# Kernel optimization log

Hardware: AMD Instinct MI355X
Metric: run time of the kernel (lower is better)

Reference implementation:

```python
import jax, jax.numpy as jnp
import numpy as np

EMBED_DIM = 512
NUM_HEADS = 8
GLOBAL_MIX = 0.5


def setup_inputs() -> dict:
    key = jax.random.key(0)
    ks = jax.random.split(key, 7)
    B, L, E = 8, 1024, EMBED_DIM
    s = 1.0 / np.sqrt(E)
    x = jax.random.normal(ks[0], (B, L, E), dtype=jnp.float32)
    mask = jax.random.randint(ks[1], (B, L), 0, 2) > 0  # True = valid token
    Wq = jax.random.normal(ks[2], (E, E), dtype=jnp.float32) * s
    Wk = jax.random.normal(ks[3], (E, E), dtype=jnp.float32) * s
    Wv = jax.random.normal(ks[4], (E, E), dtype=jnp.float32) * s
    Wo = jax.random.normal(ks[5], (E, E), dtype=jnp.float32) * s
    G = jax.random.normal(ks[6], (L, L), dtype=jnp.float32)
    return {"x": x, "mask": mask, "Wq": Wq, "Wk": Wk, "Wv": Wv, "Wo": Wo, "G": G}


def _tanh_mha(x, mask, Wq, Wk, Wv, Wo, G):
    B, L, E = x.shape
    H = NUM_HEADS
    D = E // H
    scale = 1.0 / np.sqrt(D)
    dt = x.dtype
    fmax = jnp.finfo(dt).max
    tiny = jnp.finfo(dt).tiny

    def split_heads(t):  # (B,L,E) -> (B,H,L,D)
        return t.reshape(B, L, H, D).transpose(0, 2, 1, 3)

    q = split_heads(x @ Wq.T)
    k = split_heads(x @ Wk.T)
    v = split_heads(x @ Wv.T)

    scores = jnp.tanh(jnp.einsum('bhqd,bhkd->bhqk', q, k) * scale)
    key_valid = mask[:, None, None, :]  # (B,1,1,L)
    scores = jnp.where(key_valid, scores, -jnp.inf)

    finite = jnp.isfinite(scores)
    finite_scores = jnp.where(finite, scores, -fmax)
    m = jnp.max(finite_scores, axis=(1, 2, 3), keepdims=True)  # per-sample amax over heads+q+k
    m = jnp.where(jnp.isfinite(m), m, jnp.zeros_like(m))
    exp_scores = jnp.where(finite, jnp.exp(scores - m), jnp.zeros_like(scores))

    mf = mask.astype(dt)
    exp_scores = exp_scores * mf[:, None, None, :] * mf[:, None, :, None]
    denom = jnp.maximum(exp_scores.sum(axis=(1, 2, 3), keepdims=True), tiny)
    weights = exp_scores / denom
    # dropout p=0 -> identity; renorm pass kept for faithfulness
    renorm = jnp.maximum(weights.sum(axis=(1, 2, 3), keepdims=True), tiny)
    weights = weights / renorm

    # learnable global attention: softmax rows, clamp, mask, normalize over (q,k)
    activated = jnp.maximum(jax.nn.softmax(G, axis=-1), 0.0)  # (L,L)
    gscores = activated[None] * mf[:, None, :] * mf[:, :, None]  # (B,L,L)
    gsums = jnp.maximum(gscores.sum(axis=(1, 2), keepdims=True), tiny)
    gnorm = (gscores / gsums)[:, None]  # (B,1,L,L)
    weights = (1.0 - GLOBAL_MIX) * weights + GLOBAL_MIX * gnorm

    attended = jnp.einsum('bhqk,bhkd->bhqd', weights, v)
    attended = attended * mf[:, None, :, None]
    attended = attended.transpose(0, 2, 1, 3).reshape(B, L, E)
    return attended @ Wo.T


def reference(x, mask, Wq, Wk, Wv, Wo, G):
    return _tanh_mha(x, mask, Wq, Wk, Wv, Wo, G)
```

## Files before the change

### kernel.cpp

```cpp
#include <hip/hip_runtime.h>
#include <math.h>

#define B_ 8
#define L_ 1024
#define E_ 512
#define H_ 8
#define D_ 64
#define QSZ (B_*H_*L_*D_)
#define BLE ((size_t)B_*L_*E_)
#define TINYF 1.175494350822287508e-38f
#define SWK(r) ((((r) ^ ((r) >> 3))) & 7)

typedef unsigned short u16;
typedef __attribute__((ext_vector_type(8))) short bfrag;
typedef __attribute__((ext_vector_type(4))) float ffrag;
typedef __attribute__((ext_vector_type(16))) float ffrag16;
typedef __attribute__((ext_vector_type(4))) short vshort4;

#if __has_builtin(__builtin_amdgcn_exp2f)
#define EXP2F(x) __builtin_amdgcn_exp2f(x)
#else
#define EXP2F(x) __expf((x) * 0.6931471805599453f)
#endif
#if __has_builtin(__builtin_amdgcn_rcpf)
#define RCPF(x) __builtin_amdgcn_rcpf(x)
#else
#define RCPF(x) (1.0f / (x))
#endif

__device__ __forceinline__ u16 f2b(float f) {
  unsigned u = __float_as_uint(f);
  u += 0x7fffu + ((u >> 16) & 1u);
  return (u16)(u >> 16);
}
__device__ __forceinline__ unsigned pk2(float a, float b) {
  unsigned ua = __float_as_uint(a); ua += 0x7fffu + ((ua >> 16) & 1u);
  unsigned ub = __float_as_uint(b); ub += 0x7fffu + ((ub >> 16) & 1u);
  return (ua >> 16) | (ub & 0xffff0000u);
}
__device__ __forceinline__ float blo(unsigned u) { return __uint_as_float(u << 16); }
__device__ __forceinline__ float bhi(unsigned u) { return __uint_as_float(u & 0xffff0000u); }

__device__ __forceinline__ bfrag cvt8v(const float* __restrict__ src) {
  float4 a = *(const float4*)src;
  float4 b = *(const float4*)(src + 4);
  bfrag r;
  r[0]=(short)f2b(a.x); r[1]=(short)f2b(a.y); r[2]=(short)f2b(a.z); r[3]=(short)f2b(a.w);
  r[4]=(short)f2b(b.x); r[5]=(short)f2b(b.y); r[6]=(short)f2b(b.z); r[7]=(short)f2b(b.w);
  return r;
}

__device__ __forceinline__ void gll16(const void* g, void* l) {
  __builtin_amdgcn_global_load_lds(
      (const __attribute__((address_space(1))) void*)g,
      (__attribute__((address_space(3))) void*)l, 16, 0, 0);
}

__global__ __launch_bounds__(256) void prep_softmax_k(
    const float* __restrict__ x, const float* __restrict__ Wq,
    const float* __restrict__ Wk, const float* __restrict__ Wv,
    const float* __restrict__ Wo, const float* __restrict__ G,
    const int* __restrict__ mask,
    u16* __restrict__ xb, u16* __restrict__ Wb, u16* __restrict__ actb,
    float* __restrict__ R, int* __restrict__ posb, int* __restrict__ nvb,
    int* __restrict__ itok) {
  const int bid = blockIdx.x, t = threadIdx.x;
  __shared__ float sred[8];
  __shared__ float rred[4][8];
  __shared__ int sc[256];
  if (bid < 2048) {
    size_t c = (size_t)bid * 256 + t;
    *(bfrag*)&xb[c * 8] = cvt8v(x + c * 8);
    return;
  }
  if (bid < 2560) {
    const int c2 = bid - 2048;
    const float* src = (c2 < 128) ? Wq : (c2 < 256) ? Wk : (c2 < 384) ? Wv : Wo;
    const size_t base = (size_t)(c2 >> 7) * 262144;
    const size_t cc = (size_t)(c2 & 127) * 256 + t;
    *(bfrag*)&Wb[base + cc * 8] = cvt8v(src + cc * 8);
    return;
  }
  if (bid >= 3584) {
    const int bb = bid - 3584;
    int4 mi = *(const int4*)(mask + bb * 1024 + t * 4);
    const int vx = mi.x ? 1 : 0, vy = mi.y ? 1 : 0;
    const int vz = mi.z ? 1 : 0, vw = mi.w ? 1 : 0;
    const int c0 = vx + vy + vz + vw;
    sc[t] = c0;
    __syncthreads();
#pragma unroll
    for (int off = 1; off < 256; off <<= 1) {
      int v = (t >= off) ? sc[t - off] : 0;
      __syncthreads();
      sc[t] += v;
      __syncthreads();
    }
    const int nvtot = sc[255];
    int pv = sc[t] - c0;
    int pi = t * 4 - pv;
    int4 pq;
    pq.x = vx ? pv : nvtot + pi; pv += vx; pi += 1 - vx;
    pq.y = vy ? pv : nvtot + pi; pv += vy; pi += 1 - vy;
    pq.z = vz ? pv : nvtot + pi; pv += vz; pi += 1 - vz;
    pq.w = vw ? pv : nvtot + pi;
    *(int4*)(posb + bb * 1024 + t * 4) = pq;
    itok[bb * 1024 + pq.x] = t * 4;
    itok[bb * 1024 + pq.y] = t * 4 + 1;
    itok[bb * 1024 + pq.z] = t * 4 + 2;
    itok[bb * 1024 + pq.w] = t * 4 + 3;
    if (t == 0) nvb[bb] = nvtot;
    return;
  }
  const int q = bid - 2560;
  const int w = t >> 6, lane = t & 63;
  float4 g4 = ((const float4*)(G + (size_t)q * 1024))[t];
  float m = fmaxf(fmaxf(g4.x, g4.y), fmaxf(g4.z, g4.w));
#pragma unroll
  for (int off = 32; off > 0; off >>= 1) m = fmaxf(m, __shfl_down(m, off));
  if (lane == 0) sred[w] = m;
  __syncthreads();
  m = fmaxf(fmaxf(sred[0], sred[1]), fmaxf(sred[2], sred[3]));
  float e0 = __expf(g4.x - m), e1 = __expf(g4.y - m);
  float e2 = __expf(g4.z - m), e3 = __expf(g4.w - m);
  float s = e0 + e1 + e2 + e3;
#pragma unroll
  for (int off = 32; off > 0; off >>= 1) s += __shfl_down(s, off);
  if (lane == 0) sred[4 + w] = s;
  __syncthreads();
  const float inv = 1.0f / (sred[4] + sred[5] + sred[6] + sred[7]);
  const unsigned p0 = pk2(e0 * inv, e1 * inv);
  const unsigned p1 = pk2(e2 * inv, e3 * inv);
  *(uint2*)&actb[(size_t)q * 1024 + t * 4] = make_uint2(p0, p1);
  const float r0 = blo(p0), r1 = bhi(p0);
  const float r2 = blo(p1), r3 = bhi(p1);
  float rd[8];
#pragma unroll
  for (int b = 0; b < 8; ++b) {
    const int* mkp = mask + b * 1024 + t * 4;
    rd[b] = (mkp[0] ? r0 : 0.f) + (mkp[1] ? r1 : 0.f) +
            (mkp[2] ? r2 : 0.f) + (mkp[3] ? r3 : 0.f);
#pragma unroll
    for (int off = 32; off > 0; off >>= 1) rd[b] += __shfl_down(rd[b], off);
  }
  if (lane == 0)
#pragma unroll
    for (int b = 0; b < 8; ++b) rred[w][b] = rd[b];
  __syncthreads();
  if (t < 8) R[q * 8 + t] = rred[0][t] + rred[1][t] + rred[2][t] + rred[3][t];
}

__global__ __launch_bounds__(256) void proj_k(
    const u16* __restrict__ xb, const u16* __restrict__ Wb,
    const int* __restrict__ mask, const float* __restrict__ R,
    const int* __restrict__ posb,
    float* __restrict__ sums,
    u16* __restrict__ Qb, u16* __restrict__ Kb, u16* __restrict__ Vtb) {
  const int m0 = blockIdx.x * 128;
  const int n0 = blockIdx.y * 128;
  __shared__ __align__(16) u16 As[128 * 64];
  __shared__ __align__(16) u16 Bs[128 * 64];
  __shared__ float rr[4][8];
  const int t = threadIdx.x, w = t >> 6, lane = t & 63;
  const int l15 = lane & 15, quad = lane >> 4;
  const int mq = (w >> 1) * 64, nq = (w & 1) * 64;

  if (blockIdx.x == 0 && blockIdx.y == 0) {
    float a8[8] = {0,0,0,0,0,0,0,0};
    for (int q = t; q < 1024; q += 256)
#pragma unroll
      for (int b = 0; b < 8; ++b)
        if (mask[b * 1024 + q]) a8[b] += R[q * 8 + b];
#pragma unroll
    for (int b = 0; b < 8; ++b) {
#pragma unroll
      for (int off = 32; off > 0; off >>= 1) a8[b] += __shfl_down(a8[b], off);
    }
    if (lane == 0)
#pragma unroll
      for (int b = 0; b < 8; ++b) rr[w][b] = a8[b];
    __syncthreads();
    if (t < 8) {
      sums[t] = 0.0f;
      sums[8 + t] = rr[0][t] + rr[1][t] + rr[2][t] + rr[3][t];
    }
  }

  const ffrag fz = {0.f, 0.f, 0.f, 0.f};
  ffrag acc[4][4];
#pragma unroll
  for (int i = 0; i < 4; ++i)
#pragma unroll
    for (int j = 0; j < 4; ++j) acc[i][j] = fz;

  for (int kk = 0; kk < 512; kk += 64) {
    __syncthreads();
#pragma unroll
    for (int j = 0; j < 4; ++j) {
      const int c = w * 256 + j * 64 + lane;
      const int row = c >> 3, ck = (c & 7) ^ (row & 7);
      gll16(xb + (size_t)(m0 + row) * 512 + kk + ck * 8,
            &As[(size_t)(w * 256 + j * 64) * 8]);
    }
#pragma unroll
    for (int j = 0; j < 4; ++j) {
      const int c = w * 256 + j * 64 + lane;
      const int row = c >> 3, ck = (c & 7) ^ (row & 7);
      gll16(Wb + (size_t)(n0 + row) * 512 + kk + ck * 8,
            &Bs[(size_t)(w * 256 + j * 64) * 8]);
    }
    __syncthreads();
#pragma unroll
    for (int s = 0; s < 2; ++s) {
      bfrag av[4], bv[4];
#pragma unroll
      for (int i = 0; i < 4; ++i) {
        const int ar = mq + i * 16 + l15;
        av[i] = *(const bfrag*)&As[ar * 64 + (((quad + 4 * s) ^ (ar & 7)) << 3)];
        const int br = nq + i * 16 + l15;
        bv[i] = *(const bfrag*)&Bs[br * 64 + (((quad + 4 * s) ^ (br & 7)) << 3)];
      }
#pragma unroll
      for (int i = 0; i < 4; ++i)
#pragma unroll
        for (int j = 0; j < 4; ++j)
          acc[i][j] = __builtin_amdgcn_mfma_f32_16x16x32_bf16(av[i], bv[j], acc[i][j], 0, 0, 0);
    }
  }
  const int z = n0 >> 9;
  const int c0 = n0 & 511;
#pragma unroll
  for (int i = 0; i < 4; ++i) {
    const int mbase = m0 + mq + i * 16 + quad * 4;
    const int b = mbase >> 10, l0 = mbase & 1023;
    int4 pr;
    if (z == 0) pr = *(const int4*)(posb + b * 1024 + l0);
#pragma unroll
    for (int j = 0; j < 4; ++j) {
      const int nc = c0 + nq + j * 16 + l15;
      const int h = nc >> 6, d = nc & 63;
      if (z == 0) {
        u16* dst = Qb + (size_t)(b * 8 + h) * 65536 + d;
        dst[(size_t)pr.x * 64] = f2b(acc[i][j][0]);
        dst[(size_t)pr.y * 64] = f2b(acc[i][j][1]);
        dst[(size_t)pr.z * 64] = f2b(acc[i][j][2]);
        dst[(size_t)pr.w * 64] = f2b(acc[i][j][3]);
      } else if (z == 1) {
        u16* dst = Kb + ((size_t)(b * 8 + h) * 1024 + l0) * 64 + d;
#pragma unroll
        for (int r = 0; r < 4; ++r) dst[(size_t)r * 64] = f2b(acc[i][j][r]);
      } else {
        vshort4 vs;
#pragma unroll
        for (int r = 0; r < 4; ++r)
          vs[r] = (short)(mask[b * 1024 + l0 + r] ? f2b(acc[i][j][r]) : (u16)0);
        *(vshort4*)(Vtb + ((size_t)(b * 8 + h) * 64 + d) * 1024 + l0) = vs;
      }
    }
  }
}

__global__ __launch_bounds__(256) void attn_gv_k(
    const u16* __restrict__ Qb, const u16* __restrict__ Kb,
    const u16* __restrict__ Vtb, const u16* __restrict__ actb,
    const int* __restrict__ mask, const int* __restrict__ nvb,
    const int* __restrict__ itok,
    u16* __restrict__ AEb, u16* __restrict__ AGb, float* __restrict__ denom) {
  __shared__ __align__(16) u16 POOL[13320];
  const int t = threadIdx.x, w = t >> 6, lane = t & 63;
  const int l15 = lane & 15, quad = lane >> 4;
  const int X = blockIdx.x & 7;
  const int s = blockIdx.x >> 3;
  const int s3 = s % 3, sd3 = s / 3;

  if (s3 == 2) {
    u16* As = POOL;
    u16* Bs = POOL + 4096;
    const int b = X;
    const int q0 = (sd3 >> 2) * 64;
    const int n0 = (sd3 & 3) * 128;
    const int nv = nvb[b];
    if (q0 >= nv) return;
    const int* it = itok + b * 1024;
    const int m0 = b * 1024 + q0;
    const int mq = (w >> 1) * 32, nq = (w & 1) * 64;
    const ffrag fz = {0.f, 0.f, 0.f, 0.f};
    ffrag acc[2][4];
#pragma unroll
    for (int i = 0; i < 2; ++i)
#pragma unroll
      for (int j = 0; j < 4; ++j) acc[i][j] = fz;

    int tokr[2];
#pragma unroll
    for (int j = 0; j < 2; ++j) {
      const int c = w * 128 + j * 64 + lane;
      tokr[j] = it[q0 + (c >> 3)];
    }

    for (int kk = 0; kk < 1024; kk += 64) {
      __syncthreads();
#pragma unroll
      for (int j = 0; j < 2; ++j) {
        const int c = w * 128 + j * 64 + lane;
        const int row = c >> 3, ck = (c & 7) ^ (row & 7);
        gll16(actb + (size_t)tokr[j] * 1024 + kk + ck * 8,
              &As[(size_t)(w * 128 + j * 64) * 8]);
      }
#pragma unroll
      for (int j = 0; j < 4; ++j) {
        const int c = w * 256 + j * 64 + lane;
        const int row = c >> 3, ck = (c & 7) ^ (row & 7);
        gll16(Vtb + (size_t)(b * 512 + n0 + row) * 1024 + kk + ck * 8,
              &Bs[(size_t)(w * 256 + j * 64) * 8]);
      }
      __syncthreads();
#pragma unroll
      for (int sgm = 0; sgm < 2; ++sgm) {
        bfrag av[2], bv[4];
#pragma unroll
        for (int i = 0; i < 2; ++i) {
          const int ar = mq + i * 16 + l15;
          av[i] = *(const bfrag*)&As[ar * 64 + (((quad + 4 * sgm) ^ (ar & 7)) << 3)];
        }
#pragma unroll
        for (int j = 0; j < 4; ++j) {
          const int br = nq + j * 16 + l15;
          bv[j] = *(const bfrag*)&Bs[br * 64 + (((quad + 4 * sgm) ^ (br & 7)) << 3)];
        }
#pragma unroll
        for (int i = 0; i < 2; ++i)
#pragma unroll
          for (int j = 0; j < 4; ++j)
            acc[i][j] = __builtin_amdgcn_mfma_f32_16x16x32_bf16(av[i], bv[j], acc[i][j], 0, 0, 0);
      }
    }
#pragma unroll
    for (int i = 0; i < 2; ++i) {
      const int mbase = m0 + mq + i * 16 + quad * 4;
#pragma unroll
      for (int j = 0; j < 4; ++j) {
        const int n = n0 + nq + j * 16 + l15;
#pragma unroll
        for (int r = 0; r < 4; ++r)
          AGb[(size_t)(mbase + r) * 512 + n] = f2b(acc[i][j][r]);
      }
    }
    return;
  }

  const int a_ = sd3 * 2 + s3;
  const int qt = a_ & 15;
  const int h = a_ >> 4;
  const int b = X;
  const int bh = X * 8 + h;
  const int nv = nvb[b];
  if (qt * 64 >= nv) return;
  u16* Ks = POOL;
  u16* Vs = POOL + 4096;
  u16* Es = POOL + 8192;
  u16* Ms = POOL + 12288;
  float* red4 = (float*)(POOL + 13312);
  const int l31 = lane & 31, hi = lane >> 5;
  const int qsb = w >> 1, msb = w & 1;
  const int qpb = w & 1, dpb = w >> 1;

  const u16* Kg = Kb + (size_t)bh * 65536;
  const u16* Vg = Vtb + (size_t)bh * 65536;

  const u16* Qrow = Qb + ((size_t)bh * 1024 + qt * 64 + qsb * 32 + l31) * 64;
  bfrag qf[4];
#pragma unroll
  for (int ko = 0; ko < 4; ++ko) qf[ko] = *(const bfrag*)(Qrow + ko * 16 + hi * 8);

  {
    int4 mi = *(const int4*)(mask + b * 1024 + t * 4);
    vshort4 mv;
    mv[0] = mi.x ? (short)0x3F80 : (short)0; mv[1] = mi.y ? (short)0x3F80 : (short)0;
    mv[2] = mi.z ? (short)0x3F80 : (short)0; mv[3] = mi.w ? (short)0x3F80 : (short)0;
    *(vshort4*)&Ms[t * 4] = mv;
  }

  auto stageK = [&](int kt) {
#pragma unroll
    for (int j = 0; j < 2; ++j) {
      const int c = w * 128 + j * 64 + lane;
      const int row = c >> 3, ck = (c & 7) ^ SWK(row);
      gll16(Kg + (size_t)(kt * 64 + row) * 64 + ck * 8,
            &Ks[(size_t)(w * 128 + j * 64) * 8]);
    }
  };
  auto stageV = [&](int kt) {
#pragma unroll
    for (int j = 0; j < 2; ++j) {
      const int c = w * 128 + j * 64 + lane;
      const int row = c >> 3, ck = (c & 7) ^ SWK(row);
      gll16(Vg + (size_t)row * 1024 + kt * 64 + ck * 8,
            &Vs[(size_t)(w * 128 + j * 64) * 8]);
    }
  };

  stageK(0); stageV(0);
  __syncthreads();

  ffrag16 accE, dacc;
#pragma unroll
  for (int i = 0; i < 16; ++i) { accE[i] = 0.f; dacc[i] = 0.f; }

  for (int kt = 0; kt < 16; ++kt) {
    ffrag16 st;
#pragma unroll
    for (int i = 0; i < 16; ++i) st[i] = 0.f;
    const int krow = msb * 32 + l31;
    const int kk7 = SWK(krow);
#pragma unroll
    for (int ko = 0; ko < 4; ++ko) {
      bfrag ak = *(const bfrag*)&Ks[krow * 64 + (((ko * 2 + hi) ^ kk7) << 3)];
      st = __builtin_amdgcn_mfma_f32_32x32x16_bf16(ak, qf[ko], st, 0, 0, 0);
    }
    const int qrow = qsb * 32 + l31;
    const int qk7 = SWK(qrow);
#pragma unroll
    for (int g = 0; g < 4; ++g) {
      float ee[4];
#pragma unroll
      for (int r = 0; r < 4; ++r) {
        const float tt = EXP2F(st[4 * g + r] * 0.360673760222f);
        ee[r] = EXP2F(RCPF(tt + 1.0f) * -2.88539008178f);
      }
      const int k0 = msb * 32 + g * 8 + hi * 4;
      *(uint2*)&Es[qrow * 64 + (((k0 >> 3) ^ qk7) << 3) + (k0 & 7)] =
          make_uint2(pk2(ee[0], ee[1]), pk2(ee[2], ee[3]));
    }
    __syncthreads();
    if (kt < 15) stageK(kt + 1);

    const int erow = qpb * 32 + l31;
    const int ek7 = SWK(erow);
    const int vrow = dpb * 32 + l31;
    const int vk7 = SWK(vrow);
#pragma unroll
    for (int ko = 0; ko < 4; ++ko) {
      const int co = ko * 2 + hi;
      bfrag ea = *(const bfrag*)&Es[erow * 64 + ((co ^ ek7) << 3)];
      bfrag bv = *(const bfrag*)&Vs[vrow * 64 + ((co ^ vk7) << 3)];
      accE = __builtin_amdgcn_mfma_f32_32x32x16_bf16(ea, bv, accE, 0, 0, 0);
      if (dpb == 0) {
        bfrag bm = *(const bfrag*)&Ms[kt * 64 + ko * 16 + hi * 8];
        dacc = __builtin_amdgcn_mfma_f32_32x32x16_bf16(ea, bm, dacc, 0, 0, 0);
      }
    }
    __syncthreads();
    if (kt < 15) stageV(kt + 1);
  }

  const size_t obase = ((size_t)(b * 1024 + qt * 64 + qpb * 32)) * 512
                       + h * 64 + dpb * 32 + l31;
#pragma unroll
  for (int r = 0; r < 16; ++r) {
    const int qloc = (r & 3) + 8 * (r >> 2) + 4 * hi;
    AEb[obase + (size_t)qloc * 512] = f2b(accE[r]);
  }
  float dsumv = 0.0f;
  if (l31 == 0 && dpb == 0) {
    const int cq0 = qt * 64 + qpb * 32 + 4 * hi;
#pragma unroll
    for (int r = 0; r < 16; ++r) {
      const int cq = cq0 + (r & 3) + 8 * (r >> 2);
      dsumv += (cq < nv) ? dacc[r] : 0.0f;
    }
    red4[qpb * 2 + hi] = dsumv;
  }
  __syncthreads();
  if (t == 0) atomicAdd(denom + b, red4[0] + red4[1] + red4[2] + red4[3]);
}

__global__ __launch_bounds__(256) void o_proj_k(
    const u16* __restrict__ AEb, const u16* __restrict__ AGb,
    const int* __restrict__ mask, const int* __restrict__ posb,
    const float* __restrict__ sums,
    const u16* __restrict__ Wb, float* __restrict__ out) {
  const int m0 = blockIdx.x * 128;
  const int n0 = blockIdx.y * 128;
  const int b = m0 >> 10;
  const float c1 = 0.5f / fmaxf(sums[b], TINYF);
  const float c2 = 0.5f / fmaxf(sums[8 + b], TINYF);
  __shared__ __align__(16) u16 As[128 * 64];
  __shared__ __align__(16) u16 Bs[128 * 64];
  const int t = threadIdx.x, w = t >> 6, lane = t & 63;
  const int l15 = lane & 15, quad = lane >> 4;
  const int mq = (w >> 1) * 64, nq = (w & 1) * 64;
  int rowi[4], prw[4], mrow[4]; float c1r[4], c2r[4];
#pragma unroll
  for (int i = 0; i < 4; ++i) {
    const int c = t + i * 256;
    rowi[i] = c >> 3;
    const int tok = (m0 + rowi[i]) & 1023;
    mrow[i] = mask[b * 1024 + tok];
    prw[i] = posb[b * 1024 + tok];
    c1r[i] = mrow[i] ? c1 : 0.0f;
    c2r[i] = mrow[i] ? c2 : 0.0f;
  }
  const ffrag fz = {0.f, 0.f, 0.f, 0.f};
  ffrag acc[4][4];
#pragma unroll
  for (int i = 0; i < 4; ++i)
#pragma unroll
    for (int j = 0; j < 4; ++j) acc[i][j] = fz;

  for (int kk = 0; kk < 512; kk += 64) {
    __syncthreads();
#pragma unroll
    for (int i = 0; i < 4; ++i) {
      const int c = t + i * 256;
      const int row = rowi[i], ck = c & 7;
      const size_t gofsE = (size_t)(b * 1024 + prw[i]) * 512 + kk + ck * 8;
      uint4 ua = *(const uint4*)(AEb + gofsE);
      uint4 ug = *(const uint4*)(AGb + gofsE);
      if (!mrow[i]) {
        ua = make_uint4(0u, 0u, 0u, 0u);
        ug = make_uint4(0u, 0u, 0u, 0u);
      }
      const float a1 = c1r[i], a2 = c2r[i];
      uint4 res;
      res.x = pk2(a1 * blo(ua.x) + a2 * blo(ug.x), a1 * bhi(ua.x) + a2 * bhi(ug.x));
      res.y = pk2(a1 * blo(ua.y) + a2 * blo(ug.y), a1 * bhi(ua.y) + a2 * bhi(ug.y));
      res.z = pk2(a1 * blo(ua.z) + a2 * blo(ug.z), a1 * bhi(ua.z) + a2 * bhi(ug.z));
      res.w = pk2(a1 * blo(ua.w) + a2 * blo(ug.w), a1 * bhi(ua.w) + a2 * bhi(ug.w));
      *(uint4*)&As[row * 64 + ((ck ^ (row & 7)) << 3)] = res;
    }
#pragma unroll
    for (int j = 0; j < 4; ++j) {
      const int c = w * 256 + j * 64 + lane;
      const int row = c >> 3, ck = (c & 7) ^ (row & 7);
      gll16(Wb + (size_t)(1536 + n0 + row) * 512 + kk + ck * 8,
            &Bs[(size_t)(w * 256 + j * 64) * 8]);
    }
    __syncthreads();
#pragma unroll
    for (int s = 0; s < 2; ++s) {
      bfrag av[4], bv[4];
#pragma unroll
      for (int i = 0; i < 4; ++i) {
        const int ar = mq + i * 16 + l15;
        av[i] = *(const bfrag*)&As[ar * 64 + (((quad + 4 * s) ^ (ar & 7)) << 3)];
        const int br = nq + i * 16 + l15;
        bv[i] = *(const bfrag*)&Bs[br * 64 + (((quad + 4 * s) ^ (br & 7)) << 3)];
      }
#pragma unroll
      for (int i = 0; i < 4; ++i)
#pragma unroll
        for (int j = 0; j < 4; ++j)
          acc[i][j] = __builtin_amdgcn_mfma_f32_16x16x32_bf16(av[i], bv[j], acc[i][j], 0, 0, 0);
    }
  }
#pragma unroll
  for (int i = 0; i < 4; ++i) {
    const int mbase = m0 + mq + i * 16 + quad * 4;
#pragma unroll
    for (int j = 0; j < 4; ++j) {
      const int n = n0 + nq + j * 16 + l15;
#pragma unroll
      for (int r = 0; r < 4; ++r)
        out[(size_t)(mbase + r) * 512 + n] = acc[i][j][r];
    }
  }
}

extern "C" void kernel_launch(void* const* d_in, const int* in_sizes, int n_in,
                              void* d_out, int out_size, void* d_ws, size_t ws_size,
                              hipStream_t stream) {
  const float* x  = (const float*)d_in[0];
  const int* mask = (const int*)d_in[1];
  const float* Wq = (const float*)d_in[2];
  const float* Wk = (const float*)d_in[3];
  const float* Wv = (const float*)d_in[4];
  const float* Wo = (const float*)d_in[5];
  const float* G  = (const float*)d_in[6];
  float* out = (float*)d_out;

  u16* xb   = (u16*)d_ws;
  u16* Wb   = xb + (size_t)8192 * 512;
  u16* Qb   = Wb + (size_t)2048 * 512;
  u16* Kb   = Qb + QSZ;
  u16* Vtb  = Kb + QSZ;
  u16* actb = Vtb + QSZ;
  u16* AEb  = actb + (size_t)1024 * 1024;
  u16* AGb  = AEb + BLE;
  float* R  = (float*)(AGb + BLE);
  float* SUMS = R + 8192;
  int* posb = (int*)(SUMS + 16);
  int* nvb  = posb + 8192;
  int* itok = nvb + 8;

  prep_softmax_k<<<3592, 256, 0, stream>>>(x, Wq, Wk, Wv, Wo, G, mask, xb, Wb, actb, R, posb, nvb, itok);
  proj_k<<<dim3(64, 12), 256, 0, stream>>>(xb, Wb, mask, R, posb, SUMS, Qb, Kb, Vtb);
  attn_gv_k<<<1536, 256, 0, stream>>>(Qb, Kb, Vtb, actb, mask, nvb, itok, AEb, AGb, SUMS);
  o_proj_k<<<dim3(64, 4), 256, 0, stream>>>(AEb, AGb, mask, nvb ? posb : posb, SUMS, Wb, out);
}
```

Baseline: 182.5 us.

## Gather valid query rows in Q projection and redistribute softmax work across kernels

The G-row softmax moves from the prep kernel into the projection kernel as extra blocks, and the R reduction moves into an extra block of the attention kernel. The Q projection now gathers x rows by compacted token index and skips tiles past the valid count, so Q is written contiguously in compacted order instead of scattered. The aim is to skip Q projection work for masked queries and let independent work overlap inside fewer-dependency kernels. This adds an indirect row gather and relies on Qb rows beyond nv never being read.

```diff
diff --git a/kernel.cpp b/kernel.cpp
--- a/kernel.cpp
+++ b/kernel.cpp
@@ -56,17 +56,14 @@
       (__attribute__((address_space(3))) void*)l, 16, 0, 0);
 }
 
-__global__ __launch_bounds__(256) void prep_softmax_k(
+__global__ __launch_bounds__(256) void prep_k(
     const float* __restrict__ x, const float* __restrict__ Wq,
     const float* __restrict__ Wk, const float* __restrict__ Wv,
-    const float* __restrict__ Wo, const float* __restrict__ G,
-    const int* __restrict__ mask,
-    u16* __restrict__ xb, u16* __restrict__ Wb, u16* __restrict__ actb,
-    float* __restrict__ R, int* __restrict__ posb, int* __restrict__ nvb,
-    int* __restrict__ itok) {
+    const float* __restrict__ Wo, const int* __restrict__ mask,
+    u16* __restrict__ xb, u16* __restrict__ Wb,
+    int* __restrict__ posb, int* __restrict__ nvb, int* __restrict__ itok,
+    float* __restrict__ sums) {
   const int bid = blockIdx.x, t = threadIdx.x;
-  __shared__ float sred[8];
-  __shared__ float rred[4][8];
   __shared__ int sc[256];
   if (bid < 2048) {
     size_t c = (size_t)bid * 256 + t;
@@ -81,108 +78,111 @@
     *(bfrag*)&Wb[base + cc * 8] = cvt8v(src + cc * 8);
     return;
   }
-  if (bid >= 3584) {
-    const int bb = bid - 3584;
-    int4 mi = *(const int4*)(mask + bb * 1024 + t * 4);
-    const int vx = mi.x ? 1 : 0, vy = mi.y ? 1 : 0;
-    const int vz = mi.z ? 1 : 0, vw = mi.w ? 1 : 0;
-    const int c0 = vx + vy + vz + vw;
-    sc[t] = c0;
-    __syncthreads();
-#pragma unroll
-    for (int off = 1; off < 256; off <<= 1) {
-      int v = (t >= off) ? sc[t - off] : 0;
-      __syncthreads();
-      sc[t] += v;
-      __syncthreads();
-    }
-    const int nvtot = sc[255];
-    int pv = sc[t] - c0;
-    int pi = t * 4 - pv;
-    int4 pq;
-    pq.x = vx ? pv : nvtot + pi; pv += vx; pi += 1 - vx;
-    pq.y = vy ? pv : nvtot + pi; pv += vy; pi += 1 - vy;
-    pq.z = vz ? pv : nvtot + pi; pv += vz; pi += 1 - vz;
-    pq.w = vw ? pv : nvtot + pi;
-    *(int4*)(posb + bb * 1024 + t * 4) = pq;
-    itok[bb * 1024 + pq.x] = t * 4;
-    itok[bb * 1024 + pq.y] = t * 4 + 1;
-    itok[bb * 1024 + pq.z] = t * 4 + 2;
-    itok[bb * 1024 + pq.w] = t * 4 + 3;
-    if (t == 0) nvb[bb] = nvtot;
-    return;
-  }
-  const int q = bid - 2560;
-  const int w = t >> 6, lane = t & 63;
-  float4 g4 = ((const float4*)(G + (size_t)q * 1024))[t];
-  float m = fmaxf(fmaxf(g4.x, g4.y), fmaxf(g4.z, g4.w));
-#pragma unroll
-  for (int off = 32; off > 0; off >>= 1) m = fmaxf(m, __shfl_down(m, off));
-  if (lane == 0) sred[w] = m;
+  const int bb = bid - 2560;
+  int4 mi = *(const int4*)(mask + bb * 1024 + t * 4);
+  const int vx = mi.x ? 1 : 0, vy = mi.y ? 1 : 0;
+  const int vz = mi.z ? 1 : 0, vw = mi.w ? 1 : 0;
+  const int c0 = vx + vy + vz + vw;
+  sc[t] = c0;
   __syncthreads();
-  m = fmaxf(fmaxf(sred[0], sred[1]), fmaxf(sred[2], sred[3]));
-  float e0 = __expf(g4.x - m), e1 = __expf(g4.y - m);
-  float e2 = __expf(g4.z - m), e3 = __expf(g4.w - m);
-  float s = e0 + e1 + e2 + e3;
-#pragma unroll
-  for (int off = 32; off > 0; off >>= 1) s += __shfl_down(s, off);
-  if (lane == 0) sred[4 + w] = s;
-  __syncthreads();
-  const float inv = 1.0f / (sred[4] + sred[5] + sred[6] + sred[7]);
-  const unsigned p0 = pk2(e0 * inv, e1 * inv);
-  const unsigned p1 = pk2(e2 * inv, e3 * inv);
-  *(uint2*)&actb[(size_t)q * 1024 + t * 4] = make_uint2(p0, p1);
-  const float r0 = blo(p0), r1 = bhi(p0);
-  const float r2 = blo(p1), r3 = bhi(p1);
-  float rd[8];
-#pragma unroll
-  for (int b = 0; b < 8; ++b) {
-    const int* mkp = mask + b * 1024 + t * 4;
-    rd[b] = (mkp[0] ? r0 : 0.f) + (mkp[1] ? r1 : 0.f) +
-            (mkp[2] ? r2 : 0.f) + (mkp[3] ? r3 : 0.f);
-#pragma unroll
-    for (int off = 32; off > 0; off >>= 1) rd[b] += __shfl_down(rd[b], off);
-  }
-  if (lane == 0)
-#pragma unroll
-    for (int b = 0; b < 8; ++b) rred[w][b] = rd[b];
-  __syncthreads();
-  if (t < 8) R[q * 8 + t] = rred[0][t] + rred[1][t] + rred[2][t] + rred[3][t];
+#pragma unroll
+  for (int off = 1; off < 256; off <<= 1) {
+    int v = (t >= off) ? sc[t - off] : 0;
+    __syncthreads();
+    sc[t] += v;
+    __syncthreads();
+  }
+  const int nvtot = sc[255];
+  int pv = sc[t] - c0;
+  int pi = t * 4 - pv;
+  int4 pq;
+  pq.x = vx ? pv : nvtot + pi; pv += vx; pi += 1 - vx;
+  pq.y = vy ? pv : nvtot + pi; pv += vy; pi += 1 - vy;
+  pq.z = vz ? pv : nvtot + pi; pv += vz; pi += 1 - vz;
+  pq.w = vw ? pv : nvtot + pi;
+  *(int4*)(posb + bb * 1024 + t * 4) = pq;
+  itok[bb * 1024 + pq.x] = t * 4;
+  itok[bb * 1024 + pq.y] = t * 4 + 1;
+  itok[bb * 1024 + pq.z] = t * 4 + 2;
+  itok[bb * 1024 + pq.w] = t * 4 + 3;
+  if (t == 0) { nvb[bb] = nvtot; sums[bb] = 0.0f; }
 }
 
 __global__ __launch_bounds__(256) void proj_k(
     const u16* __restrict__ xb, const u16* __restrict__ Wb,
-    const int* __restrict__ mask, const float* __restrict__ R,
-    const int* __restrict__ posb,
-    float* __restrict__ sums,
+    const float* __restrict__ G, const int* __restrict__ mask,
+    const int* __restrict__ nvb, const int* __restrict__ itok,
+    u16* __restrict__ actb, float* __restrict__ R,
     u16* __restrict__ Qb, u16* __restrict__ Kb, u16* __restrict__ Vtb) {
-  const int m0 = blockIdx.x * 128;
-  const int n0 = blockIdx.y * 128;
+  const int bid = blockIdx.x, t = threadIdx.x;
   __shared__ __align__(16) u16 As[128 * 64];
   __shared__ __align__(16) u16 Bs[128 * 64];
-  __shared__ float rr[4][8];
-  const int t = threadIdx.x, w = t >> 6, lane = t & 63;
+  __shared__ float sred[8];
+  __shared__ float rred[4][8];
+  const int w = t >> 6, lane = t & 63;
+
+  if (bid < 1024) {
+    const int q = bid;
+    float4 g4 = ((const float4*)(G + (size_t)q * 1024))[t];
+    float m = fmaxf(fmaxf(g4.x, g4.y), fmaxf(g4.z, g4.w));
+#pragma unroll
+    for (int off = 32; off > 0; off >>= 1) m = fmaxf(m, __shfl_down(m, off));
+    if (lane == 0) sred[w] = m;
+    __syncthreads();
+    m = fmaxf(fmaxf(sred[0], sred[1]), fmaxf(sred[2], sred[3]));
+    float e0 = __expf(g4.x - m), e1 = __expf(g4.y - m);
+    float e2 = __expf(g4.z - m), e3 = __expf(g4.w - m);
+    float s = e0 + e1 + e2 + e3;
+#pragma unroll
+    for (int off = 32; off > 0; off >>= 1) s += __shfl_down(s, off);
+    if (lane == 0) sred[4 + w] = s;
+    __syncthreads();
+    const float inv = 1.0f / (sred[4] + sred[5] + sred[6] + sred[7]);
+    const unsigned p0 = pk2(e0 * inv, e1 * inv);
+    const unsigned p1 = pk2(e2 * inv, e3 * inv);
+    *(uint2*)&actb[(size_t)q * 1024 + t * 4] = make_uint2(p0, p1);
+    const float r0 = blo(p0), r1 = bhi(p0);
+    const float r2 = blo(p1), r3 = bhi(p1);
+    float rd[8];
+#pragma unroll
+    for (int b = 0; b < 8; ++b) {
+      const int* mkp = mask + b * 1024 + t * 4;
+      rd[b] = (mkp[0] ? r0 : 0.f) + (mkp[1] ? r1 : 0.f) +
+              (mkp[2] ? r2 : 0.f) + (mkp[3] ? r3 : 0.f);
+#pragma unroll
+      for (int off = 32; off > 0; off >>= 1) rd[b] += __shfl_down(rd[b], off);
+    }
+    if (lane == 0)
+#pragma unroll
+      for (int b = 0; b < 8; ++b) rred[w][b] = rd[b];
+    __syncthreads();
+    if (t < 8) R[q * 8 + t] = rred[0][t] + rred[1][t] + rred[2][t] + rred[3][t];
+    return;
+  }
+
+  const int gid = bid - 1024;
+  const int m0 = (gid & 63) * 128;
+  const int n0 = (gid >> 6) * 128;
   const int l15 = lane & 15, quad = lane >> 4;
   const int mq = (w >> 1) * 64, nq = (w & 1) * 64;
-
-  if (blockIdx.x == 0 && blockIdx.y == 0) {
-    float a8[8] = {0,0,0,0,0,0,0,0};
-    for (int q = t; q < 1024; q += 256)
-#pragma unroll
-      for (int b = 0; b < 8; ++b)
-        if (mask[b * 1024 + q]) a8[b] += R[q * 8 + b];
-#pragma unroll
-    for (int b = 0; b < 8; ++b) {
-#pragma unroll
-      for (int off = 32; off > 0; off >>= 1) a8[b] += __shfl_down(a8[b], off);
-    }
-    if (lane == 0)
-#pragma unroll
-      for (int b = 0; b < 8; ++b) rr[w][b] = a8[b];
-    __syncthreads();
-    if (t < 8) {
-      sums[t] = 0.0f;
-      sums[8 + t] = rr[0][t] + rr[1][t] + rr[2][t] + rr[3][t];
+  const int z = n0 >> 9;
+  const int b = m0 >> 10, q0c = m0 & 1023;
+
+  int tokr[4];
+  if (z == 0) {
+    const int nv = nvb[b];
+    if (q0c >= nv) return;
+    const int* it = itok + b * 1024;
+#pragma unroll
+    for (int j = 0; j < 4; ++j) {
+      const int c = w * 256 + j * 64 + lane;
+      tokr[j] = b * 1024 + it[q0c + (c >> 3)];
+    }
+  } else {
+#pragma unroll
+    for (int j = 0; j < 4; ++j) {
+      const int c = w * 256 + j * 64 + lane;
+      tokr[j] = m0 + (c >> 3);
     }
   }
 
@@ -199,7 +199,7 @@
     for (int j = 0; j < 4; ++j) {
       const int c = w * 256 + j * 64 + lane;
       const int row = c >> 3, ck = (c & 7) ^ (row & 7);
-      gll16(xb + (size_t)(m0 + row) * 512 + kk + ck * 8,
+      gll16(xb + (size_t)tokr[j] * 512 + kk + ck * 8,
             &As[(size_t)(w * 256 + j * 64) * 8]);
     }
 #pragma unroll
@@ -227,24 +227,19 @@
           acc[i][j] = __builtin_amdgcn_mfma_f32_16x16x32_bf16(av[i], bv[j], acc[i][j], 0, 0, 0);
     }
   }
-  const int z = n0 >> 9;
   const int c0 = n0 & 511;
 #pragma unroll
   for (int i = 0; i < 4; ++i) {
     const int mbase = m0 + mq + i * 16 + quad * 4;
-    const int b = mbase >> 10, l0 = mbase & 1023;
-    int4 pr;
-    if (z == 0) pr = *(const int4*)(posb + b * 1024 + l0);
+    const int l0 = mbase & 1023;
 #pragma unroll
     for (int j = 0; j < 4; ++j) {
       const int nc = c0 + nq + j * 16 + l15;
       const int h = nc >> 6, d = nc & 63;
       if (z == 0) {
-        u16* dst = Qb + (size_t)(b * 8 + h) * 65536 + d;
-        dst[(size_t)pr.x * 64] = f2b(acc[i][j][0]);
-        dst[(size_t)pr.y * 64] = f2b(acc[i][j][1]);
-        dst[(size_t)pr.z * 64] = f2b(acc[i][j][2]);
-        dst[(size_t)pr.w * 64] = f2b(acc[i][j][3]);
+        u16* dst = Qb + ((size_t)(b * 8 + h) * 1024 + l0) * 64 + d;
+#pragma unroll
+        for (int r = 0; r < 4; ++r) dst[(size_t)r * 64] = f2b(acc[i][j][r]);
       } else if (z == 1) {
         u16* dst = Kb + ((size_t)(b * 8 + h) * 1024 + l0) * 64 + d;
 #pragma unroll
@@ -264,11 +259,32 @@
     const u16* __restrict__ Qb, const u16* __restrict__ Kb,
     const u16* __restrict__ Vtb, const u16* __restrict__ actb,
     const int* __restrict__ mask, const int* __restrict__ nvb,
-    const int* __restrict__ itok,
+    const int* __restrict__ itok, const float* __restrict__ R,
     u16* __restrict__ AEb, u16* __restrict__ AGb, float* __restrict__ denom) {
   __shared__ __align__(16) u16 POOL[13320];
   const int t = threadIdx.x, w = t >> 6, lane = t & 63;
   const int l15 = lane & 15, quad = lane >> 4;
+
+  if (blockIdx.x == 1536) {
+    float* rr = (float*)POOL;
+    float a8[8] = {0,0,0,0,0,0,0,0};
+    for (int q = t; q < 1024; q += 256)
+#pragma unroll
+      for (int b = 0; b < 8; ++b)
+        if (mask[b * 1024 + q]) a8[b] += R[q * 8 + b];
+#pragma unroll
+    for (int b = 0; b < 8; ++b) {
+#pragma unroll
+      for (int off = 32; off > 0; off >>= 1) a8[b] += __shfl_down(a8[b], off);
+    }
+    if (lane == 0)
+#pragma unroll
+      for (int b = 0; b < 8; ++b) rr[w * 8 + b] = a8[b];
+    __syncthreads();
+    if (t < 8) denom[8 + t] = rr[t] + rr[8 + t] + rr[16 + t] + rr[24 + t];
+    return;
+  }
+
   const int X = blockIdx.x & 7;
   const int s = blockIdx.x >> 3;
   const int s3 = s % 3, sd3 = s / 3;
@@ -593,8 +609,8 @@
   int* nvb  = posb + 8192;
   int* itok = nvb + 8;
 
-  prep_softmax_k<<<3592, 256, 0, stream>>>(x, Wq, Wk, Wv, Wo, G, mask, xb, Wb, actb, R, posb, nvb, itok);
-  proj_k<<<dim3(64, 12), 256, 0, stream>>>(xb, Wb, mask, R, posb, SUMS, Qb, Kb, Vtb);
-  attn_gv_k<<<1536, 256, 0, stream>>>(Qb, Kb, Vtb, actb, mask, nvb, itok, AEb, AGb, SUMS);
-  o_proj_k<<<dim3(64, 4), 256, 0, stream>>>(AEb, AGb, mask, nvb ? posb : posb, SUMS, Wb, out);
-}
+  prep_k<<<2568, 256, 0, stream>>>(x, Wq, Wk, Wv, Wo, mask, xb, Wb, posb, nvb, itok, SUMS);
+  proj_k<<<1792, 256, 0, stream>>>(xb, Wb, G, mask, nvb, itok, actb, R, Qb, Kb, Vtb);
+  attn_gv_k<<<1537, 256, 0, stream>>>(Qb, Kb, Vtb, actb, mask, nvb, itok, R, AEb, AGb, SUMS);
+  o_proj_k<<<dim3(64, 4), 256, 0, stream>>>(AEb, AGb, mask, posb, SUMS, Wb, out);
+}
```

After: 173.9 us. -4.7%, faster.
